# Kernel optimization log

Hardware: AMD Instinct MI355X
Metric: run time of the kernel (lower is better)

The kernel has to match this reference:

```python
import jax, jax.numpy as jnp
import numpy as np

N_NODES = 100000


def _gcn_norm(edge_index, n):
    # Add self loops and compute symmetric normalization deg^-1/2 A_hat deg^-1/2
    loops = jnp.arange(n, dtype=edge_index.dtype)
    row = jnp.concatenate([edge_index[0], loops])  # source nodes [E+N]
    col = jnp.concatenate([edge_index[1], loops])  # target nodes [E+N]
    ones = jnp.ones(row.shape[0], dtype=jnp.float32)
    deg = jax.ops.segment_sum(ones, col, num_segments=n)  # in-degree incl. self loop
    dinv = jnp.where(deg > 0, jax.lax.rsqrt(deg), 0.0)
    norm = dinv[row] * dinv[col]  # [E+N]
    return row, col, norm


def _gcn_conv(x, W, b, row, col, norm, n):
    h = x @ W                     # [N, out]
    msg = h[row] * norm[:, None]  # gather + scale  [E+N, out]
    agg = jax.ops.segment_sum(msg, col, num_segments=n)  # scatter-add
    return agg + b


def setup_inputs() -> dict:
    key = jax.random.key(0)
    ks = jax.random.split(key, 8)
    n, e, din, dh, dout = N_NODES, 1600000, 128, 128, 64
    x = jax.random.normal(ks[0], (n, din), dtype=jnp.float32)
    edge_index = jax.random.randint(ks[1], (2, e), 0, n, dtype=jnp.int64)
    s = lambda fan: 1.0 / np.sqrt(fan)
    W0 = jax.random.normal(ks[2], (din, dh), dtype=jnp.float32) * s(din)
    W1 = jax.random.normal(ks[3], (dh, dh), dtype=jnp.float32) * s(dh)
    W2 = jax.random.normal(ks[4], (dh, dout), dtype=jnp.float32) * s(dh)
    b0 = jnp.zeros((dh,), jnp.float32)
    b1 = jnp.zeros((dh,), jnp.float32)
    b2 = jnp.zeros((dout,), jnp.float32)
    return {"x": x, "edge_index": edge_index, "W0": W0, "b0": b0,
            "W1": W1, "b1": b1, "W2": W2, "b2": b2}


def reference(x, edge_index, W0, b0, W1, b1, W2, b2):
    # Eval-mode forward (dropout inactive), matching GCN.forward
    n = x.shape[0]
    row, col, norm = _gcn_norm(edge_index, n)
    h = jax.nn.relu(_gcn_conv(x, W0, b0, row, col, norm, n))
    h = jax.nn.relu(_gcn_conv(h, W1, b1, row, col, norm, n))
    out = _gcn_conv(h, W2, b2, row, col, norm, n)
    return out
```

## Files before the change

kernel.cpp:

```cpp
#include <hip/hip_runtime.h>
#include <stdint.h>


static inline size_t ws_align(size_t x) { return (x + 255) & ~(size_t)255; }

typedef float __f2 __attribute__((ext_vector_type(2)));
typedef float __f4 __attribute__((ext_vector_type(4)));
typedef __attribute__((ext_vector_type(8))) short short8v;
typedef __attribute__((ext_vector_type(4))) float f32x4;

__device__ __forceinline__ int eidx(const void* p, size_t i, int is64) {
  return is64 ? (int)((const long long*)p)[i] : ((const int*)p)[i];
}

__device__ __forceinline__ uint16_t f2bf(float f) {
  uint32_t u = __float_as_uint(f);
  u += 0x7fffu + ((u >> 16) & 1u);
  return (uint16_t)(u >> 16);
}
__device__ __forceinline__ float bf_lo(uint32_t h) { return __uint_as_float(h << 16); }
__device__ __forceinline__ float bf_hi(uint32_t h) { return __uint_as_float(h & 0xffff0000u); }

__global__ void detect_k(const int* ei, int* flag) {
  int l = threadIdx.x;
  int v = ei[2 * l + 1];
  unsigned long long m = __ballot(v == 0);
  if (l == 0) *flag = (m == ~0ULL) ? 1 : 0;
}

__global__ __launch_bounds__(256) void passA_k(const void* ei, const int* __restrict__ flag,
                                               int* __restrict__ bucket_cnt, int E, int NB) {
  __shared__ int cnt[256];
  int t = threadIdx.x;
  cnt[t] = 0;
  __syncthreads();
  int is64 = *flag;
  for (int e = blockIdx.x * 256 + t; e < E; e += gridDim.x * 256) {
    int c = eidx(ei, (size_t)E + e, is64);
    atomicAdd(&cnt[c >> 9], 1);
  }
  __syncthreads();
  if (t < NB && cnt[t]) atomicAdd(&bucket_cnt[t], cnt[t]);
}

__global__ __launch_bounds__(256) void bscan_k(const int* __restrict__ bucket_cnt,
                                               int* __restrict__ bucket_offs,
                                               int* __restrict__ gcursor, int NB) {
  __shared__ int sh[256];
  int t = threadIdx.x;
  int v = (t < NB) ? bucket_cnt[t] : 0;
  sh[t] = v;
  __syncthreads();
  for (int off = 1; off < 256; off <<= 1) {
    int x = (t >= off) ? sh[t - off] : 0;
    __syncthreads();
    sh[t] += x;
    __syncthreads();
  }
  if (t < NB) {
    int excl = sh[t] - v;
    bucket_offs[t] = excl;
    gcursor[t] = excl;
  }
  if (t == NB - 1) bucket_offs[NB] = sh[t];
}

__global__ __launch_bounds__(512) void passB_k(const void* ei, const int* __restrict__ flag,
                                               int* __restrict__ gcursor,
                                               int2* __restrict__ epk_binned, int E, int NB) {
  __shared__ int2 sorted[4096];
  __shared__ int cnt[256], bbase[256], gb[256], cur[256];
  __shared__ int sh[256];
  const int t = threadIdx.x;
  const int base = blockIdx.x * 4096;
  const int CH = min(4096, E - base);
  const int is64 = *flag;

  if (t < 256) cnt[t] = 0;
  __syncthreads();
  for (int i = t; i < CH; i += 512) {
    int c = eidx(ei, (size_t)E + base + i, is64);
    atomicAdd(&cnt[c >> 9], 1);
  }
  __syncthreads();
  if (t < 256) sh[t] = cnt[t];
  __syncthreads();
  for (int off = 1; off < 256; off <<= 1) {
    int x = (t < 256 && t >= off) ? sh[t - off] : 0;
    __syncthreads();
    if (t < 256) sh[t] += x;
    __syncthreads();
  }
  if (t < 256) {
    int v = cnt[t];
    bbase[t] = sh[t] - v;
    gb[t] = (t < NB && v) ? atomicAdd(&gcursor[t], v) : 0;
    cur[t] = 0;
  }
  __syncthreads();
  for (int i = t; i < CH; i += 512) {
    int r = eidx(ei, (size_t)base + i, is64);
    int c = eidx(ei, (size_t)E + base + i, is64);
    int b = c >> 9;
    int rank = atomicAdd(&cur[b], 1);
    sorted[bbase[b] + rank] = make_int2(r, c);
  }
  __syncthreads();
  for (int i = t; i < CH; i += 512) {
    int2 v = sorted[i];
    int b = v.y >> 9;
    epk_binned[gb[b] + (i - bbase[b])] = v;
  }
}

__global__ __launch_bounds__(1024) void passC0_k(const int2* __restrict__ epk_binned,
                                                 const int* __restrict__ bucket_offs,
                                                 int* __restrict__ deg, int* __restrict__ offs,
                                                 int n, int NB) {
  __shared__ int dcnt[512];
  __shared__ int s[512];
  const int t = threadIdx.x;
  const int b = blockIdx.x;
  if (t < 512) dcnt[t] = 0;
  __syncthreads();
  const int lo = bucket_offs[b], hi = bucket_offs[b + 1];
  for (int i = lo + t; i < hi; i += 1024)
    atomicAdd(&dcnt[epk_binned[i].y & 511], 1);
  __syncthreads();
  int v = (t < 512) ? dcnt[t] : 0;
  if (t < 512) s[t] = v;
  __syncthreads();
  for (int off = 1; off < 512; off <<= 1) {
    int x = (t < 512 && t >= off) ? s[t - off] : 0;
    __syncthreads();
    if (t < 512) s[t] += x;
    __syncthreads();
  }
  if (t < 512) {
    int g = (b << 9) + t;
    if (g < n) { deg[g] = v; offs[g] = lo + (s[t] - v); }
  }
  if (b == NB - 1 && t == 0) offs[n] = hi;
}

__global__ void dinv_k(const int* __restrict__ deg, float* __restrict__ dinv, int n) {
  int i = blockIdx.x * blockDim.x + threadIdx.x;
  if (i < n) dinv[i] = rsqrtf((float)deg[i] + 1.0f);
}

__global__ __launch_bounds__(1024) void passC_k(const int2* __restrict__ epk_binned,
                                                const int* __restrict__ bucket_offs,
                                                const int* __restrict__ offs,
                                                uint32_t* __restrict__ epk) {
  __shared__ int cur[512];
  const int t = threadIdx.x;
  const int b = blockIdx.x;
  if (t < 512) cur[t] = 0;
  __syncthreads();
  const int lo = bucket_offs[b], hi = bucket_offs[b + 1];
  for (int i = lo + t; i < hi; i += 1024) {
    int2 v = epk_binned[i];
    int pos = offs[v.y] + atomicAdd(&cur[v.y & 511], 1);
    epk[pos] = (uint32_t)v.x;
  }
}

template <int COLS>
__global__ void wprep_k(const float* __restrict__ W, uint16_t* __restrict__ Wf) {
  constexpr int CT = COLS / 16;
  const int f = blockIdx.x;
  const int kc = f / CT, ct = f % CT;
  const int l = threadIdx.x;
#pragma unroll
  for (int j = 0; j < 8; ++j) {
    int k = kc * 32 + (l >> 4) * 8 + j;
    int col = ct * 16 + (l & 15);
    float wv = W[(size_t)k * COLS + col];
    uint16_t hi = f2bf(wv);
    float res = wv - __uint_as_float((uint32_t)hi << 16);
    Wf[(size_t)f * 1024 + l * 8 + j] = hi;
    Wf[(size_t)f * 1024 + 512 + l * 8 + j] = f2bf(res);
  }
}

template <int COLS, bool SLICED_IN>
__global__ __launch_bounds__(256) void gemm_k(const float* __restrict__ X,
                                              const uint16_t* __restrict__ Wf,
                                              const float* __restrict__ dinv,
                                              uint16_t* __restrict__ H, int N) {
  constexpr int CT = COLS / 16;
  __shared__ uint32_t Xp[128 * 32];

  const int tid = threadIdx.x;
  const int l = tid & 63, w = tid >> 6;
  const int rowbase = blockIdx.x * 128;
  const float4* X4 = (const float4*)X;

  f32x4 acc[2][CT];
#pragma unroll
  for (int rt = 0; rt < 2; ++rt)
#pragma unroll
    for (int ct = 0; ct < CT; ++ct) acc[rt][ct] = (f32x4)0.f;

  for (int kc = 0; kc < 4; ++kc) {
    __syncthreads();
#pragma unroll
    for (int t = 0; t < 4; ++t) {
      int i = tid + t * 256;
      int r = i >> 3, q = i & 7;
      int gr = rowbase + r;
      if (gr >= N) gr = N - 1;
      float4 xv;
      if (SLICED_IN) {
        xv = X4[((size_t)kc * N + gr) * 8 + q];
      } else {
        xv = X4[(size_t)gr * 32 + kc * 8 + q];
      }
      float xs[4] = {xv.x, xv.y, xv.z, xv.w};
      uint32_t p[4];
#pragma unroll
      for (int e = 0; e < 4; ++e) {
        uint16_t hi = f2bf(xs[e]);
        float res = xs[e] - __uint_as_float((uint32_t)hi << 16);
        p[e] = ((uint32_t)hi << 16) | (uint32_t)f2bf(res);
      }
      int blk = q ^ (r & 7);
      *(uint4*)&Xp[r * 32 + blk * 4] = make_uint4(p[0], p[1], p[2], p[3]);
    }
    __syncthreads();

    short8v ah[2], al[2];
#pragma unroll
    for (int rt = 0; rt < 2; ++rt) {
      int r = w * 32 + rt * 16 + (l & 15);
      int c = (r & 7) << 2;
      int b0 = ((l >> 4) * 8) ^ c;
      int b1 = ((l >> 4) * 8 + 4) ^ c;
      uint32_t ua[8];
      *(uint4*)&ua[0] = *(const uint4*)&Xp[r * 32 + b0];
      *(uint4*)&ua[4] = *(const uint4*)&Xp[r * 32 + b1];
      union { uint32_t d[4]; short8v v; } ch, cl;
#pragma unroll
      for (int p2 = 0; p2 < 4; ++p2) {
        ch.d[p2] = __builtin_amdgcn_perm(ua[2 * p2 + 1], ua[2 * p2], 0x07060302u);
        cl.d[p2] = __builtin_amdgcn_perm(ua[2 * p2 + 1], ua[2 * p2], 0x05040100u);
      }
      ah[rt] = ch.v;
      al[rt] = cl.v;
    }

#pragma unroll
    for (int ct = 0; ct < CT; ++ct) {
      size_t fo = (size_t)(kc * CT + ct) * 1024;
      short8v bh = *(const short8v*)(Wf + fo + l * 8);
      short8v bl = *(const short8v*)(Wf + fo + 512 + l * 8);
#pragma unroll
      for (int rt = 0; rt < 2; ++rt) {
        acc[rt][ct] = __builtin_amdgcn_mfma_f32_16x16x32_bf16(ah[rt], bh, acc[rt][ct], 0, 0, 0);
        acc[rt][ct] = __builtin_amdgcn_mfma_f32_16x16x32_bf16(al[rt], bh, acc[rt][ct], 0, 0, 0);
        acc[rt][ct] = __builtin_amdgcn_mfma_f32_16x16x32_bf16(ah[rt], bl, acc[rt][ct], 0, 0, 0);
      }
    }
  }

  uint32_t* HW = (uint32_t*)H;
  const int lq = l >> 4, lc = l & 15;
#pragma unroll
  for (int rt = 0; rt < 2; ++rt) {
#pragma unroll
    for (int q = 0; q < 4; ++q) {
      int row = rowbase + w * 32 + rt * 16 + lq * 4 + q;
      bool ok = row < N;
      float dv = ok ? dinv[row] : 0.f;
#pragma unroll
      for (int ct = 0; ct < CT; ++ct) {
        float v = acc[rt][ct][q] * dv;
        int b = (int)f2bf(v);
        int other = __shfl_xor(b, 1);
        if (ok && !(l & 1)) {
          uint32_t word = (uint32_t)b | ((uint32_t)other << 16);
          HW[((size_t)(ct >> 1) * N + row) * 16 + (ct & 1) * 8 + (lc >> 1)] = word;
        }
      }
    }
  }
}

__global__ __launch_bounds__(256, 8) void agg128s_k(const uint32_t* __restrict__ HW,
                                                    const int* __restrict__ offs,
                                                    const uint32_t* __restrict__ epk,
                                                    const float* __restrict__ bias,
                                                    float* __restrict__ Aout,
                                                    int relu, int N) {
  const int s = blockIdx.x & 3;
  const int g = blockIdx.x >> 2;
  const int lane = threadIdx.x & 63;
  const int wid = threadIdx.x >> 6;
  const int d = lane >> 3, w = lane & 7;
  const int c = g * 32 + wid * 8 + d;
  if (c >= N) return;
  const uint32_t* Hs = HW + (size_t)s * N * 16;
  int e0 = offs[c], e1 = offs[c + 1];
  float a0 = 0.f, a1 = 0.f, a2 = 0.f, a3 = 0.f;
  int e = e0;
  for (; e + 8 <= e1; e += 8) {
    uint32_t p0 = epk[e],     p1 = epk[e + 1], p2 = epk[e + 2], p3 = epk[e + 3];
    uint32_t p4 = epk[e + 4], p5 = epk[e + 5], p6 = epk[e + 6], p7 = epk[e + 7];
    uint2 h0 = *(const uint2*)&Hs[(size_t)p0 * 16 + 2 * w];
    uint2 h1 = *(const uint2*)&Hs[(size_t)p1 * 16 + 2 * w];
    uint2 h2 = *(const uint2*)&Hs[(size_t)p2 * 16 + 2 * w];
    uint2 h3 = *(const uint2*)&Hs[(size_t)p3 * 16 + 2 * w];
    uint2 h4 = *(const uint2*)&Hs[(size_t)p4 * 16 + 2 * w];
    uint2 h5 = *(const uint2*)&Hs[(size_t)p5 * 16 + 2 * w];
    uint2 h6 = *(const uint2*)&Hs[(size_t)p6 * 16 + 2 * w];
    uint2 h7 = *(const uint2*)&Hs[(size_t)p7 * 16 + 2 * w];
    a0 += bf_lo(h0.x); a1 += bf_hi(h0.x); a2 += bf_lo(h0.y); a3 += bf_hi(h0.y);
    a0 += bf_lo(h1.x); a1 += bf_hi(h1.x); a2 += bf_lo(h1.y); a3 += bf_hi(h1.y);
    a0 += bf_lo(h2.x); a1 += bf_hi(h2.x); a2 += bf_lo(h2.y); a3 += bf_hi(h2.y);
    a0 += bf_lo(h3.x); a1 += bf_hi(h3.x); a2 += bf_lo(h3.y); a3 += bf_hi(h3.y);
    a0 += bf_lo(h4.x); a1 += bf_hi(h4.x); a2 += bf_lo(h4.y); a3 += bf_hi(h4.y);
    a0 += bf_lo(h5.x); a1 += bf_hi(h5.x); a2 += bf_lo(h5.y); a3 += bf_hi(h5.y);
    a0 += bf_lo(h6.x); a1 += bf_hi(h6.x); a2 += bf_lo(h6.y); a3 += bf_hi(h6.y);
    a0 += bf_lo(h7.x); a1 += bf_hi(h7.x); a2 += bf_lo(h7.y); a3 += bf_hi(h7.y);
  }
  for (; e + 4 <= e1; e += 4) {
    uint32_t p0 = epk[e], p1 = epk[e + 1], p2 = epk[e + 2], p3 = epk[e + 3];
    uint2 h0 = *(const uint2*)&Hs[(size_t)p0 * 16 + 2 * w];
    uint2 h1 = *(const uint2*)&Hs[(size_t)p1 * 16 + 2 * w];
    uint2 h2 = *(const uint2*)&Hs[(size_t)p2 * 16 + 2 * w];
    uint2 h3 = *(const uint2*)&Hs[(size_t)p3 * 16 + 2 * w];
    a0 += bf_lo(h0.x); a1 += bf_hi(h0.x); a2 += bf_lo(h0.y); a3 += bf_hi(h0.y);
    a0 += bf_lo(h1.x); a1 += bf_hi(h1.x); a2 += bf_lo(h1.y); a3 += bf_hi(h1.y);
    a0 += bf_lo(h2.x); a1 += bf_hi(h2.x); a2 += bf_lo(h2.y); a3 += bf_hi(h2.y);
    a0 += bf_lo(h3.x); a1 += bf_hi(h3.x); a2 += bf_lo(h3.y); a3 += bf_hi(h3.y);
  }
  for (; e < e1; ++e) {
    uint2 h = *(const uint2*)&Hs[(size_t)epk[e] * 16 + 2 * w];
    a0 += bf_lo(h.x); a1 += bf_hi(h.x); a2 += bf_lo(h.y); a3 += bf_hi(h.y);
  }
  float dc = rsqrtf((float)(e1 - e0) + 1.f);
  uint2 hc = *(const uint2*)&Hs[(size_t)c * 16 + 2 * w];
  float r0 = fmaf(dc, a0 + bf_lo(hc.x), bias[s * 32 + 4 * w + 0]);
  float r1 = fmaf(dc, a1 + bf_hi(hc.x), bias[s * 32 + 4 * w + 1]);
  float r2 = fmaf(dc, a2 + bf_lo(hc.y), bias[s * 32 + 4 * w + 2]);
  float r3 = fmaf(dc, a3 + bf_hi(hc.y), bias[s * 32 + 4 * w + 3]);
  if (relu) {
    r0 = fmaxf(r0, 0.f); r1 = fmaxf(r1, 0.f);
    r2 = fmaxf(r2, 0.f); r3 = fmaxf(r3, 0.f);
  }
  __f4 res; res.x = r0; res.y = r1; res.z = r2; res.w = r3;
  __builtin_nontemporal_store(res, (__f4*)(Aout + ((size_t)s * N + c) * 32 + 4 * w));
}

__global__ __launch_bounds__(256, 8) void agg64s_k(const uint32_t* __restrict__ HW,
                                                   const int* __restrict__ offs,
                                                   const uint32_t* __restrict__ epk,
                                                   const float* __restrict__ bias,
                                                   float* __restrict__ out, int N) {
  const int r = blockIdx.x & 7;
  const int s = r >> 2;
  const int quar = r & 3;
  const int ng = (N + 31) >> 5;
  const int nq = (ng + 3) >> 2;
  const int g = quar * nq + (blockIdx.x >> 3);
  if (g >= ng) return;
  const int lane = threadIdx.x & 63;
  const int wid = threadIdx.x >> 6;
  const int d = lane >> 3, w = lane & 7;
  const int c = g * 32 + wid * 8 + d;
  if (c >= N) return;
  const uint32_t* Hs = HW + (size_t)s * N * 16;
  int e0 = offs[c], e1 = offs[c + 1];
  float a0 = 0.f, a1 = 0.f, a2 = 0.f, a3 = 0.f;
  int e = e0;
  for (; e + 8 <= e1; e += 8) {
    uint32_t p0 = epk[e],     p1 = epk[e + 1], p2 = epk[e + 2], p3 = epk[e + 3];
    uint32_t p4 = epk[e + 4], p5 = epk[e + 5], p6 = epk[e + 6], p7 = epk[e + 7];
    uint2 h0 = *(const uint2*)&Hs[(size_t)p0 * 16 + 2 * w];
    uint2 h1 = *(const uint2*)&Hs[(size_t)p1 * 16 + 2 * w];
    uint2 h2 = *(const uint2*)&Hs[(size_t)p2 * 16 + 2 * w];
    uint2 h3 = *(const uint2*)&Hs[(size_t)p3 * 16 + 2 * w];
    uint2 h4 = *(const uint2*)&Hs[(size_t)p4 * 16 + 2 * w];
    uint2 h5 = *(const uint2*)&Hs[(size_t)p5 * 16 + 2 * w];
    uint2 h6 = *(const uint2*)&Hs[(size_t)p6 * 16 + 2 * w];
    uint2 h7 = *(const uint2*)&Hs[(size_t)p7 * 16 + 2 * w];
    a0 += bf_lo(h0.x); a1 += bf_hi(h0.x); a2 += bf_lo(h0.y); a3 += bf_hi(h0.y);
    a0 += bf_lo(h1.x); a1 += bf_hi(h1.x); a2 += bf_lo(h1.y); a3 += bf_hi(h1.y);
    a0 += bf_lo(h2.x); a1 += bf_hi(h2.x); a2 += bf_lo(h2.y); a3 += bf_hi(h2.y);
    a0 += bf_lo(h3.x); a1 += bf_hi(h3.x); a2 += bf_lo(h3.y); a3 += bf_hi(h3.y);
    a0 += bf_lo(h4.x); a1 += bf_hi(h4.x); a2 += bf_lo(h4.y); a3 += bf_hi(h4.y);
    a0 += bf_lo(h5.x); a1 += bf_hi(h5.x); a2 += bf_lo(h5.y); a3 += bf_hi(h5.y);
    a0 += bf_lo(h6.x); a1 += bf_hi(h6.x); a2 += bf_lo(h6.y); a3 += bf_hi(h6.y);
    a0 += bf_lo(h7.x); a1 += bf_hi(h7.x); a2 += bf_lo(h7.y); a3 += bf_hi(h7.y);
  }
  for (; e + 4 <= e1; e += 4) {
    uint32_t p0 = epk[e], p1 = epk[e + 1], p2 = epk[e + 2], p3 = epk[e + 3];
    uint2 h0 = *(const uint2*)&Hs[(size_t)p0 * 16 + 2 * w];
    uint2 h1 = *(const uint2*)&Hs[(size_t)p1 * 16 + 2 * w];
    uint2 h2 = *(const uint2*)&Hs[(size_t)p2 * 16 + 2 * w];
    uint2 h3 = *(const uint2*)&Hs[(size_t)p3 * 16 + 2 * w];
    a0 += bf_lo(h0.x); a1 += bf_hi(h0.x); a2 += bf_lo(h0.y); a3 += bf_hi(h0.y);
    a0 += bf_lo(h1.x); a1 += bf_hi(h1.x); a2 += bf_lo(h1.y); a3 += bf_hi(h1.y);
    a0 += bf_lo(h2.x); a1 += bf_hi(h2.x); a2 += bf_lo(h2.y); a3 += bf_hi(h2.y);
    a0 += bf_lo(h3.x); a1 += bf_hi(h3.x); a2 += bf_lo(h3.y); a3 += bf_hi(h3.y);
  }
  for (; e < e1; ++e) {
    uint2 h = *(const uint2*)&Hs[(size_t)epk[e] * 16 + 2 * w];
    a0 += bf_lo(h.x); a1 += bf_hi(h.x); a2 += bf_lo(h.y); a3 += bf_hi(h.y);
  }
  float dc = rsqrtf((float)(e1 - e0) + 1.f);
  uint2 hc = *(const uint2*)&Hs[(size_t)c * 16 + 2 * w];
  float r0 = fmaf(dc, a0 + bf_lo(hc.x), bias[s * 32 + 4 * w + 0]);
  float r1 = fmaf(dc, a1 + bf_hi(hc.x), bias[s * 32 + 4 * w + 1]);
  float r2 = fmaf(dc, a2 + bf_lo(hc.y), bias[s * 32 + 4 * w + 2]);
  float r3 = fmaf(dc, a3 + bf_hi(hc.y), bias[s * 32 + 4 * w + 3]);
  __f4 res; res.x = r0; res.y = r1; res.z = r2; res.w = r3;
  __builtin_nontemporal_store(res, (__f4*)(out + (size_t)c * 64 + s * 32 + 4 * w));
}

extern "C" void kernel_launch(void* const* d_in, const int* in_sizes, int n_in,
                              void* d_out, int out_size, void* d_ws, size_t ws_size,
                              hipStream_t stream) {
  const float* x  = (const float*)d_in[0];
  const void*  ei = d_in[1];
  const float* W0 = (const float*)d_in[2];
  const float* b0 = (const float*)d_in[3];
  const float* W1 = (const float*)d_in[4];
  const float* b1 = (const float*)d_in[5];
  const float* W2 = (const float*)d_in[6];
  const float* b2 = (const float*)d_in[7];
  float* out = (float*)d_out;

  const int n = in_sizes[0] / 128;
  const int E = in_sizes[1] / 2;
  const int NB = (n + 511) >> 9;

  char* ws = (char*)d_ws;
  size_t off = 0;
  auto alloc = [&](size_t bytes) { char* p = ws + off; off = ws_align(off + bytes); return p; };
  int*      bucket_cnt  = (int*)alloc(256 * 4);
  int*      bucket_offs = (int*)alloc(257 * 4);
  int*      gcursor     = (int*)alloc(256 * 4);
  int*      deg         = (int*)alloc((size_t)n * 4);
  int*      offs        = (int*)alloc((size_t)(n + 1) * 4);
  float*    dinv        = (float*)alloc((size_t)n * 4);
  int*      flag        = (int*)alloc(4);
  uint16_t* wf0         = (uint16_t*)alloc(64 * 1024);
  uint16_t* wf1         = (uint16_t*)alloc(64 * 1024);
  uint16_t* wf2         = (uint16_t*)alloc(32 * 1024);
  int2*     epk_binned  = (int2*)alloc((size_t)E * 8);
  uint32_t* epk         = (uint32_t*)alloc((size_t)E * 4);
  uint16_t* hbuf        = (uint16_t*)alloc((size_t)n * 128 * 2);
  float*    abuf        = (float*)alloc((size_t)n * 128 * 4);
  (void)ws_size;

  hipMemsetAsync(bucket_cnt, 0, 256 * 4, stream);

  wprep_k<128><<<32, 64, 0, stream>>>(W0, wf0);
  wprep_k<128><<<32, 64, 0, stream>>>(W1, wf1);
  wprep_k<64><<<16, 64, 0, stream>>>(W2, wf2);

  detect_k<<<1, 64, 0, stream>>>((const int*)ei, flag);
  passA_k<<<1024, 256, 0, stream>>>(ei, flag, bucket_cnt, E, NB);
  bscan_k<<<1, 256, 0, stream>>>(bucket_cnt, bucket_offs, gcursor, NB);
  passB_k<<<(E + 4095) / 4096, 512, 0, stream>>>(ei, flag, gcursor, epk_binned, E, NB);
  passC0_k<<<NB, 1024, 0, stream>>>(epk_binned, bucket_offs, deg, offs, n, NB);
  dinv_k<<<(n + 255) / 256, 256, 0, stream>>>(deg, dinv, n);
  passC_k<<<NB, 1024, 0, stream>>>(epk_binned, bucket_offs, offs, epk);

  const int gemm_blocks = (n + 127) / 128;
  const int agg128_blocks = 4 * ((n + 31) / 32);
  const int ng = (n + 31) >> 5, nq = (ng + 3) >> 2;
  const int agg64_blocks = 8 * nq;

  gemm_k<128, false><<<gemm_blocks, 256, 0, stream>>>(x, wf0, dinv, hbuf, n);
  agg128s_k<<<agg128_blocks, 256, 0, stream>>>((const uint32_t*)hbuf, offs, epk, b0, abuf, 1, n);
  gemm_k<128, true><<<gemm_blocks, 256, 0, stream>>>(abuf, wf1, dinv, hbuf, n);
  agg128s_k<<<agg128_blocks, 256, 0, stream>>>((const uint32_t*)hbuf, offs, epk, b1, abuf, 1, n);
  gemm_k<64, true><<<gemm_blocks, 256, 0, stream>>>(abuf, wf2, dinv, hbuf, n);
  agg64s_k<<<agg64_blocks, 256, 0, stream>>>((const uint32_t*)hbuf, offs, epk, b2, out, n);
}
```

Measured before the change: 425.0 us.

## Store hidden activations as bf16 and pack binned edges into 32 bits

The aggregation kernel now writes its intermediate activations as bf16 instead of fp32. The following GEMM reads them directly and skips the low-residual MFMA pass, since bf16 inputs have no residual. Edge binning packs the source index with the local 9-bit target offset into one uint32, halving the binned-edge traffic. The passB write-out becomes a per-bucket serial copy loop, which may coalesce worse. Rounding intermediates to bf16 adds precision loss, and the packed shift assumes source indices fit in 23 bits.

```diff
diff --git a/kernel.cpp b/kernel.cpp
--- a/kernel.cpp
+++ b/kernel.cpp
@@ -6,6 +6,7 @@
 
 typedef float __f2 __attribute__((ext_vector_type(2)));
 typedef float __f4 __attribute__((ext_vector_type(4)));
+typedef uint32_t __u2 __attribute__((ext_vector_type(2)));
 typedef __attribute__((ext_vector_type(8))) short short8v;
 typedef __attribute__((ext_vector_type(4))) float f32x4;
 
@@ -67,8 +68,8 @@
 
 __global__ __launch_bounds__(512) void passB_k(const void* ei, const int* __restrict__ flag,
                                                int* __restrict__ gcursor,
-                                               int2* __restrict__ epk_binned, int E, int NB) {
-  __shared__ int2 sorted[4096];
+                                               uint32_t* __restrict__ epk_binned, int E, int NB) {
+  __shared__ uint32_t sorted[4096];
   __shared__ int cnt[256], bbase[256], gb[256], cur[256];
   __shared__ int sh[256];
   const int t = threadIdx.x;
@@ -103,17 +104,20 @@
     int c = eidx(ei, (size_t)E + base + i, is64);
     int b = c >> 9;
     int rank = atomicAdd(&cur[b], 1);
-    sorted[bbase[b] + rank] = make_int2(r, c);
+    sorted[bbase[b] + rank] = ((uint32_t)r << 9) | (uint32_t)(c & 511);
   }
   __syncthreads();
   for (int i = t; i < CH; i += 512) {
-    int2 v = sorted[i];
-    int b = v.y >> 9;
-    epk_binned[gb[b] + (i - bbase[b])] = v;
-  }
-}
-
-__global__ __launch_bounds__(1024) void passC0_k(const int2* __restrict__ epk_binned,
+    ;
+  }
+  for (int b = t; b < 256; b += 512) {
+    int lo = bbase[b], c0 = cnt[b], g0 = gb[b];
+    for (int j = 0; j < c0; ++j)
+      epk_binned[g0 + j] = sorted[lo + j];
+  }
+}
+
+__global__ __launch_bounds__(1024) void passC0_k(const uint32_t* __restrict__ epk_binned,
                                                  const int* __restrict__ bucket_offs,
                                                  int* __restrict__ deg, int* __restrict__ offs,
                                                  int n, int NB) {
@@ -125,7 +129,7 @@
   __syncthreads();
   const int lo = bucket_offs[b], hi = bucket_offs[b + 1];
   for (int i = lo + t; i < hi; i += 1024)
-    atomicAdd(&dcnt[epk_binned[i].y & 511], 1);
+    atomicAdd(&dcnt[epk_binned[i] & 511u], 1);
   __syncthreads();
   int v = (t < 512) ? dcnt[t] : 0;
   if (t < 512) s[t] = v;
@@ -148,7 +152,7 @@
   if (i < n) dinv[i] = rsqrtf((float)deg[i] + 1.0f);
 }
 
-__global__ __launch_bounds__(1024) void passC_k(const int2* __restrict__ epk_binned,
+__global__ __launch_bounds__(1024) void passC_k(const uint32_t* __restrict__ epk_binned,
                                                 const int* __restrict__ bucket_offs,
                                                 const int* __restrict__ offs,
                                                 uint32_t* __restrict__ epk) {
@@ -158,10 +162,12 @@
   if (t < 512) cur[t] = 0;
   __syncthreads();
   const int lo = bucket_offs[b], hi = bucket_offs[b + 1];
+  const int node0 = b << 9;
   for (int i = lo + t; i < hi; i += 1024) {
-    int2 v = epk_binned[i];
-    int pos = offs[v.y] + atomicAdd(&cur[v.y & 511], 1);
-    epk[pos] = (uint32_t)v.x;
+    uint32_t v = epk_binned[i];
+    int dl = (int)(v & 511u);
+    int pos = offs[node0 + dl] + atomicAdd(&cur[dl], 1);
+    epk[pos] = v >> 9;
   }
 }
 
@@ -184,7 +190,7 @@
 }
 
 template <int COLS, bool SLICED_IN>
-__global__ __launch_bounds__(256) void gemm_k(const float* __restrict__ X,
+__global__ __launch_bounds__(256) void gemm_k(const void* __restrict__ Xv,
                                               const uint16_t* __restrict__ Wf,
                                               const float* __restrict__ dinv,
                                               uint16_t* __restrict__ H, int N) {
@@ -194,7 +200,6 @@
   const int tid = threadIdx.x;
   const int l = tid & 63, w = tid >> 6;
   const int rowbase = blockIdx.x * 128;
-  const float4* X4 = (const float4*)X;
 
   f32x4 acc[2][CT];
 #pragma unroll
@@ -210,19 +215,24 @@
       int r = i >> 3, q = i & 7;
       int gr = rowbase + r;
       if (gr >= N) gr = N - 1;
-      float4 xv;
+      uint32_t p[4];
       if (SLICED_IN) {
-        xv = X4[((size_t)kc * N + gr) * 8 + q];
+        const uint32_t* XW = (const uint32_t*)Xv;
+        uint2 wv = *(const uint2*)&XW[((size_t)kc * N + gr) * 16 + 2 * q];
+        p[0] = wv.x << 16;
+        p[1] = wv.x & 0xffff0000u;
+        p[2] = wv.y << 16;
+        p[3] = wv.y & 0xffff0000u;
       } else {
-        xv = X4[(size_t)gr * 32 + kc * 8 + q];
-      }
-      float xs[4] = {xv.x, xv.y, xv.z, xv.w};
-      uint32_t p[4];
-#pragma unroll
-      for (int e = 0; e < 4; ++e) {
-        uint16_t hi = f2bf(xs[e]);
-        float res = xs[e] - __uint_as_float((uint32_t)hi << 16);
-        p[e] = ((uint32_t)hi << 16) | (uint32_t)f2bf(res);
+        const float4* X4 = (const float4*)Xv;
+        float4 xv = X4[(size_t)gr * 32 + kc * 8 + q];
+        float xs[4] = {xv.x, xv.y, xv.z, xv.w};
+#pragma unroll
+        for (int e = 0; e < 4; ++e) {
+          uint16_t hi = f2bf(xs[e]);
+          float res = xs[e] - __uint_as_float((uint32_t)hi << 16);
+          p[e] = ((uint32_t)hi << 16) | (uint32_t)f2bf(res);
+        }
       }
       int blk = q ^ (r & 7);
       *(uint4*)&Xp[r * 32 + blk * 4] = make_uint4(p[0], p[1], p[2], p[3]);
@@ -243,10 +253,11 @@
 #pragma unroll
       for (int p2 = 0; p2 < 4; ++p2) {
         ch.d[p2] = __builtin_amdgcn_perm(ua[2 * p2 + 1], ua[2 * p2], 0x07060302u);
-        cl.d[p2] = __builtin_amdgcn_perm(ua[2 * p2 + 1], ua[2 * p2], 0x05040100u);
+        if (!SLICED_IN)
+          cl.d[p2] = __builtin_amdgcn_perm(ua[2 * p2 + 1], ua[2 * p2], 0x05040100u);
       }
       ah[rt] = ch.v;
-      al[rt] = cl.v;
+      if (!SLICED_IN) al[rt] = cl.v;
     }
 
 #pragma unroll
@@ -257,7 +268,8 @@
 #pragma unroll
       for (int rt = 0; rt < 2; ++rt) {
         acc[rt][ct] = __builtin_amdgcn_mfma_f32_16x16x32_bf16(ah[rt], bh, acc[rt][ct], 0, 0, 0);
-        acc[rt][ct] = __builtin_amdgcn_mfma_f32_16x16x32_bf16(al[rt], bh, acc[rt][ct], 0, 0, 0);
+        if (!SLICED_IN)
+          acc[rt][ct] = __builtin_amdgcn_mfma_f32_16x16x32_bf16(al[rt], bh, acc[rt][ct], 0, 0, 0);
         acc[rt][ct] = __builtin_amdgcn_mfma_f32_16x16x32_bf16(ah[rt], bl, acc[rt][ct], 0, 0, 0);
       }
     }
@@ -290,7 +302,7 @@
                                                     const int* __restrict__ offs,
                                                     const uint32_t* __restrict__ epk,
                                                     const float* __restrict__ bias,
-                                                    float* __restrict__ Aout,
+                                                    uint32_t* __restrict__ Aout,
                                                     int relu, int N) {
   const int s = blockIdx.x & 3;
   const int g = blockIdx.x >> 2;
@@ -348,8 +360,10 @@
     r0 = fmaxf(r0, 0.f); r1 = fmaxf(r1, 0.f);
     r2 = fmaxf(r2, 0.f); r3 = fmaxf(r3, 0.f);
   }
-  __f4 res; res.x = r0; res.y = r1; res.z = r2; res.w = r3;
-  __builtin_nontemporal_store(res, (__f4*)(Aout + ((size_t)s * N + c) * 32 + 4 * w));
+  uint32_t w0 = (uint32_t)f2bf(r0) | ((uint32_t)f2bf(r1) << 16);
+  uint32_t w1 = (uint32_t)f2bf(r2) | ((uint32_t)f2bf(r3) << 16);
+  __u2 res; res.x = w0; res.y = w1;
+  __builtin_nontemporal_store(res, (__u2*)(Aout + ((size_t)s * N + c) * 16 + 2 * w));
 }
 
 __global__ __launch_bounds__(256, 8) void agg64s_k(const uint32_t* __restrict__ HW,
@@ -448,10 +462,10 @@
   uint16_t* wf0         = (uint16_t*)alloc(64 * 1024);
   uint16_t* wf1         = (uint16_t*)alloc(64 * 1024);
   uint16_t* wf2         = (uint16_t*)alloc(32 * 1024);
-  int2*     epk_binned  = (int2*)alloc((size_t)E * 8);
+  uint32_t* epk_binned  = (uint32_t*)alloc((size_t)E * 4);
   uint32_t* epk         = (uint32_t*)alloc((size_t)E * 4);
   uint16_t* hbuf        = (uint16_t*)alloc((size_t)n * 128 * 2);
-  float*    abuf        = (float*)alloc((size_t)n * 128 * 4);
+  uint32_t* abuf        = (uint32_t*)alloc((size_t)n * 128 * 2);
   (void)ws_size;
 
   hipMemsetAsync(bucket_cnt, 0, 256 * 4, stream);
```

Result: no change. 418.5 us (-1.5%).
